# Kernel tuning notes

Measured on AMD Instinct MI355X. Metric: run time of the kernel, lower is better.

## Reference

```python
import jax, jax.numpy as jnp
import numpy as np

B, G = 64, 48            # events, grid side -> N = B*G*G nodes
N = B * G * G
DIMS = [128, 102, 73, 44, 16]   # channel schedule from GraphZ defaults
KERN = 3                 # GMM kernels on the conv layer
MAXV = 1.0               # Cartesian(max_value=neighbors=1)


def _build_graph():
    # 3x3 window graph (radius 1, self loops) per event, as in window_edges
    ix, iy = np.meshgrid(np.arange(G), np.arange(G), indexing='ij')
    ix, iy = ix.ravel(), iy.ravel()
    srcs, tgts = [], []
    for dx in (-1, 0, 1):
        for dy in (-1, 0, 1):
            jx, jy = ix + dx, iy + dy
            m = (jx >= 0) & (jx < G) & (jy >= 0) & (jy < G)
            srcs.append(jx[m] * G + jy[m])
            tgts.append(ix[m] * G + iy[m])
    src, tgt = np.concatenate(srcs), np.concatenate(tgts)
    base = (np.arange(B) * G * G)[:, None]
    ei = np.stack([(base + src[None]).ravel(), (base + tgt[None]).ravel()])
    pos = np.stack([np.tile(ix, B).astype(np.float32),
                    np.tile(iy, B).astype(np.float32),
                    np.repeat(np.arange(B), G * G).astype(np.float32)], axis=1)
    return ei.astype(np.int32), pos


def setup_inputs() -> dict:
    key = jax.random.key(0)
    ks = jax.random.split(key, 16)
    ei, pos = _build_graph()
    inp = {
        'x': jax.random.normal(ks[0], (N, DIMS[0]), jnp.float32),
        'pos': jnp.asarray(pos),
        'edge_index': jnp.asarray(ei),
    }
    # pointwise layer 0: 128->102 (+BN)
    inp['w0'] = jax.random.normal(ks[1], (DIMS[0], DIMS[1]), jnp.float32) * (1.0 / np.sqrt(DIMS[0]))
    inp['b0'] = jnp.zeros((DIMS[1],), jnp.float32)
    inp['gamma0'] = jnp.ones((DIMS[1],), jnp.float32)
    inp['beta0'] = jnp.zeros((DIMS[1],), jnp.float32)
    # pointwise layer 1: 102->73 (+BN)
    inp['w1'] = jax.random.normal(ks[2], (DIMS[1], DIMS[2]), jnp.float32) * (1.0 / np.sqrt(DIMS[1]))
    inp['b1'] = jnp.zeros((DIMS[2],), jnp.float32)
    inp['gamma1'] = jnp.ones((DIMS[2],), jnp.float32)
    inp['beta1'] = jnp.zeros((DIMS[2],), jnp.float32)
    # GMM conv layer 2: 73->44, 3 gaussian kernels (+BN)
    inp['w2'] = jax.random.normal(ks[3], (DIMS[2], DIMS[3]), jnp.float32) * (1.0 / np.sqrt(DIMS[2]))
    inp['g2'] = jax.random.normal(ks[4], (DIMS[2], KERN * DIMS[3]), jnp.float32) * (1.0 / np.sqrt(DIMS[2]))
    inp['mu2'] = jax.random.uniform(ks[5], (KERN, 2), jnp.float32)
    inp['sigma2'] = jax.random.uniform(ks[6], (KERN, 2), jnp.float32) + 0.5
    inp['b2'] = jnp.zeros((DIMS[3],), jnp.float32)
    inp['gamma2'] = jnp.ones((DIMS[3],), jnp.float32)
    inp['beta2'] = jnp.zeros((DIMS[3],), jnp.float32)
    # pointwise layer 3: 44->16
    inp['w3'] = jax.random.normal(ks[7], (DIMS[3], DIMS[4]), jnp.float32) * (1.0 / np.sqrt(DIMS[3]))
    inp['b3'] = jnp.zeros((DIMS[4],), jnp.float32)
    return inp


def _bn(x, gamma, beta):
    # BatchNorm1d training forward: biased batch stats over the node dim
    m = jnp.mean(x, axis=0)
    v = jnp.mean((x - m) ** 2, axis=0)
    return (x - m) * jax.lax.rsqrt(v + 1e-5) * gamma + beta


def _gmm_conv(x, ei, ea, g, mu, sigma, w_root, b, n):
    # PyG GMMConv (separate_gaussians=False, aggr='mean', root_weight, bias)
    E = ea.shape[0]
    kk = mu.shape[0]
    out = w_root.shape[1]
    xj = (x @ g)[ei[0]].reshape(E, kk, out)                 # gather transformed src feats
    gauss = jnp.exp(jnp.sum(-0.5 * (ea[:, None, :] - mu[None]) ** 2
                            / (1e-15 + sigma[None] ** 2), axis=-1))  # [E, K]
    msg = jnp.einsum('eko,ek->eo', xj, gauss)               # [E, out]
    s = jax.ops.segment_sum(msg, ei[1], num_segments=n)     # scatter-add to targets
    c = jax.ops.segment_sum(jnp.ones((E,), x.dtype), ei[1], num_segments=n)
    return s / jnp.maximum(c, 1.0)[:, None] + x @ w_root + b


def reference(x, pos, edge_index, w0, b0, gamma0, beta0, w1, b1, gamma1, beta1,
              w2, g2, mu2, sigma2, b2, gamma2, beta2, w3, b3):
    n = x.shape[0]
    pos2 = pos[:, :2]
    # Cartesian(max_value=1, norm=True): pseudo coords in [0, 1]
    ea = (pos2[edge_index[0]] - pos2[edge_index[1]]) / (2.0 * MAXV) + 0.5
    # layers 0,1: knn_graph(k=0) -> empty edge set -> GMMConv = root Linear + bias
    h = _bn(x @ w0 + b0, gamma0, beta0)
    h = _bn(h @ w1 + b1, gamma1, beta1)
    # layer 2: window-edge GMMConv with 3 gaussian kernels
    h = _bn(_gmm_conv(h, edge_index, ea, g2, mu2, sigma2, w2, b2, n), gamma2, beta2)
    # layer 3: pointwise, no norm
    return h @ w3 + b3
```

## Files before the change

### kernel.cpp

```cpp
#include <hip/hip_runtime.h>

#define GRIDW 48
#define NNODES 147456
#define NTILES 2304
#define GB 512

typedef __attribute__((ext_vector_type(8))) short short8;
typedef __attribute__((ext_vector_type(4))) float f32x4;
typedef __attribute__((ext_vector_type(4))) unsigned short ushort4v;

__device__ inline unsigned short f2bf(float f) {
    union { float f; unsigned u; } v; v.f = f;
    unsigned r = v.u + 0x7FFFu + ((v.u >> 16) & 1u);
    return (unsigned short)(r >> 16);
}
__device__ inline float bf2f(unsigned short h) {
    union { unsigned u; float f; } v; v.u = ((unsigned)h) << 16;
    return v.f;
}

__global__ void prep(const float* __restrict__ w0, const float* __restrict__ b0,
                     const float* __restrict__ w1, const float* __restrict__ b1,
                     const float* __restrict__ g2, const float* __restrict__ w2,
                     const float* __restrict__ b2, const float* __restrict__ w3,
                     const float* __restrict__ b3,
                     unsigned short* __restrict__ wt0, unsigned short* __restrict__ wt1,
                     unsigned short* __restrict__ wt2, unsigned short* __restrict__ wt3,
                     float* __restrict__ biasf0, float* __restrict__ biasf1,
                     float* __restrict__ biasf2, float* __restrict__ biasf3,
                     float* __restrict__ statz) {
    int id = blockIdx.x * 256 + threadIdx.x;
    if (id < 14336) {
        int col = id >> 7, k = id & 127;
        wt0[id] = (col < 102) ? f2bf(w0[k * 102 + col]) : (unsigned short)0;
    } else if (id < 24576) {
        int e = id - 14336; int col = e >> 7, k = e & 127;
        wt1[e] = (col < 73 && k < 102) ? f2bf(w1[k * 73 + col]) : (unsigned short)0;
    } else if (id < 41472) {
        int e = id - 24576; int col = e / 96, k = e - (e / 96) * 96;
        unsigned short v = 0;
        if (k < 73) v = (col < 132) ? f2bf(g2[k * 132 + col]) : f2bf(w2[k * 44 + (col - 132)]);
        wt2[e] = v;
    } else if (id < 42496) {
        int e = id - 41472; int col = e >> 6, k = e & 63;
        wt3[e] = (k < 44) ? f2bf(w3[k * 16 + col]) : (unsigned short)0;
    } else if (id < 42608) { int c = id - 42496; biasf0[c] = (c < 102) ? b0[c] : 0.f; }
    else if (id < 42688) { int c = id - 42608; biasf1[c] = (c < 73) ? b1[c] : 0.f; }
    else if (id < 42864) { int c = id - 42688; biasf2[c] = (c < 132) ? 0.f : b2[c - 132]; }
    else if (id < 42880) { int c = id - 42864; biasf3[c] = b3[c]; }
    else if (id < 43392) { statz[id - 42880] = 0.f; }
}

template<int K, int KP, int MP, int MOUT, int PREVM, int BNSRC,
         bool STATS, bool OUTBF, bool ABF16>
__global__ __launch_bounds__(256) void gemm_p(
    const void* __restrict__ Ain, const unsigned short* __restrict__ WT,
    const float* __restrict__ biasf,
    const float* __restrict__ q0, const float* __restrict__ q1,
    const float* __restrict__ q2, const float* __restrict__ q3,
    float invN, void* __restrict__ Yout,
    float* __restrict__ sumO, float* __restrict__ ssO)
{
    constexpr int KS = KP + 8;
    constexpr int NCF = MP / 16;
    constexpr int UPR = ABF16 ? (K / 8) : (K / 4);
    constexpr int TOT = 64 * UPR;
    constexpr int NLD = (TOT + 255) / 256;
    __shared__ __align__(16) unsigned short As[2][64 * KS];
    __shared__ __align__(16) unsigned short Bs[MP * KS];
    __shared__ float bnA[KP], bnB[KP];

    const int tid = threadIdx.x;
    const int lane = tid & 63, wv = tid >> 6, qd = lane >> 4, lc = lane & 15;

    if (BNSRC == 1) {
        if (tid < KP) {
            float a = 0.f, b = 0.f;
            if (tid < PREVM) {
                float m = q0[tid] * invN;
                float v = q1[tid] * invN - m * m;
                float sc = q2[tid] * rsqrtf(v + 1e-5f);
                a = sc; b = q3[tid] - m * sc;
            }
            bnA[tid] = a; bnB[tid] = b;
        }
    } else if (BNSRC == 2) {
        if (tid < KP) {
            bnA[tid] = (tid < PREVM) ? q0[tid] : 0.f;
            bnB[tid] = (tid < PREVM) ? q1[tid] : 0.f;
        }
    }
    for (int g = tid; g < MP * (KP / 8); g += 256) {
        int col = g / (KP / 8), u = g - col * (KP / 8);
        *(uint4*)&Bs[col * KS + u * 8] = *(const uint4*)&WT[(size_t)col * KP + u * 8];
    }
    if constexpr (KP > K) {
        constexpr int PADU = (KP - K) / 2;
        for (int g = tid; g < 64 * PADU; g += 256) {
            int row = g / PADU, u = g - row * PADU;
            *(unsigned*)&As[0][row * KS + K + u * 2] = 0u;
            *(unsigned*)&As[1][row * KS + K + u * 2] = 0u;
        }
    }

    float bvr[NCF];
#pragma unroll
    for (int cf = 0; cf < NCF; ++cf) bvr[cf] = biasf[cf * 16 + lc];

    float cs[NCF], cq[NCF];
    if (STATS) {
#pragma unroll
        for (int cf = 0; cf < NCF; ++cf) { cs[cf] = 0.f; cq[cf] = 0.f; }
    }

    uint4 pfb[NLD];
    float4 pff[NLD];

    int t = blockIdx.x;
#pragma unroll
    for (int i = 0; i < NLD; ++i) {
        int g = tid + 256 * i;
        if (g < TOT) {
            if constexpr (ABF16)
                pfb[i] = *(const uint4*)((const unsigned short*)Ain + (size_t)t * 64 * K + g * 8);
            else
                pff[i] = *(const float4*)((const float*)Ain + (size_t)t * 64 * K + g * 4);
        }
    }
    __syncthreads();

    int buf = 0;
    for (; t < NTILES; t += GB) {
#pragma unroll
        for (int i = 0; i < NLD; ++i) {
            int g = tid + 256 * i;
            if (g < TOT) {
                int row = g / UPR, u = g - row * UPR;
                if constexpr (ABF16) {
                    uint4 w = pfb[i];
                    if (BNSRC != 0) {
                        unsigned* wp = (unsigned*)&w;
#pragma unroll
                        for (int pp = 0; pp < 4; ++pp) {
                            int kk = u * 8 + 2 * pp;
                            float lo = bf2f((unsigned short)(wp[pp] & 0xFFFFu)) * bnA[kk] + bnB[kk];
                            float hi = bf2f((unsigned short)(wp[pp] >> 16)) * bnA[kk + 1] + bnB[kk + 1];
                            wp[pp] = (unsigned)f2bf(lo) | ((unsigned)f2bf(hi) << 16);
                        }
                    }
                    *(uint4*)&As[buf][row * KS + u * 8] = w;
                } else {
                    float4 v = pff[i];
                    if (BNSRC != 0) {
                        int kk = u * 4;
                        v.x = v.x * bnA[kk] + bnB[kk];
                        v.y = v.y * bnA[kk + 1] + bnB[kk + 1];
                        v.z = v.z * bnA[kk + 2] + bnB[kk + 2];
                        v.w = v.w * bnA[kk + 3] + bnB[kk + 3];
                    }
                    unsigned lo = (unsigned)f2bf(v.x) | ((unsigned)f2bf(v.y) << 16);
                    unsigned hi = (unsigned)f2bf(v.z) | ((unsigned)f2bf(v.w) << 16);
                    *(uint2*)&As[buf][row * KS + u * 4] = make_uint2(lo, hi);
                }
            }
        }
        int t2 = t + GB;
        if (t2 < NTILES) {
#pragma unroll
            for (int i = 0; i < NLD; ++i) {
                int g = tid + 256 * i;
                if (g < TOT) {
                    if constexpr (ABF16)
                        pfb[i] = *(const uint4*)((const unsigned short*)Ain + (size_t)t2 * 64 * K + g * 8);
                    else
                        pff[i] = *(const float4*)((const float*)Ain + (size_t)t2 * 64 * K + g * 4);
                }
            }
        }
        __syncthreads();

        f32x4 acc[NCF];
#pragma unroll
        for (int cf = 0; cf < NCF; ++cf) acc[cf] = (f32x4){0.f, 0.f, 0.f, 0.f};
#pragma unroll
        for (int kt = 0; kt < KP / 32; ++kt) {
            const int kb = kt * 32 + qd * 8;
            short8 a = *(const short8*)&As[buf][(wv * 16 + lc) * KS + kb];
#pragma unroll
            for (int cf = 0; cf < NCF; ++cf) {
                short8 b = *(const short8*)&Bs[(cf * 16 + lc) * KS + kb];
                acc[cf] = __builtin_amdgcn_mfma_f32_16x16x32_bf16(a, b, acc[cf], 0, 0, 0);
            }
        }
#pragma unroll
        for (int cf = 0; cf < NCF; ++cf) {
            const int col = cf * 16 + lc;
            const float bv = bvr[cf];
#pragma unroll
            for (int rr = 0; rr < 4; ++rr) {
                float v = acc[cf][rr] + bv;
                int row = t * 64 + wv * 16 + qd * 4 + rr;
                if (OUTBF) ((unsigned short*)Yout)[(size_t)row * MP + col] = f2bf(v);
                else       ((float*)Yout)[(size_t)row * MP + col] = v;
                if (STATS) { cs[cf] += v; cq[cf] += v * v; }
            }
        }
        buf ^= 1;
    }

    if (STATS) {
        __syncthreads();
        float* red = (float*)As;
        float* redq = red + 4 * MP;
#pragma unroll
        for (int cf = 0; cf < NCF; ++cf) {
            float s = cs[cf], qq = cq[cf];
            s += __shfl_down(s, 32, 64); s += __shfl_down(s, 16, 64);
            qq += __shfl_down(qq, 32, 64); qq += __shfl_down(qq, 16, 64);
            if (lane < 16) {
                red[wv * MP + cf * 16 + lane] = s;
                redq[wv * MP + cf * 16 + lane] = qq;
            }
        }
        __syncthreads();
        if (tid < MOUT) {
            float s = red[tid] + red[MP + tid] + red[2 * MP + tid] + red[3 * MP + tid];
            float qq = redq[tid] + redq[MP + tid] + redq[2 * MP + tid] + redq[3 * MP + tid];
            atomicAdd(&sumO[tid], s);
            atomicAdd(&ssO[tid], qq);
        }
    }
}

__global__ __launch_bounds__(256) void gmm_stencil(
    const unsigned short* __restrict__ TR, unsigned short* __restrict__ C,
    const float* __restrict__ mu, const float* __restrict__ sigma,
    float* __restrict__ sum2, float* __restrict__ ss2)
{
    __shared__ float gs[9][3];
    __shared__ float red[88];
    const int tid = threadIdx.x;
    if (tid < 88) red[tid] = 0.f;
    if (tid < 27) {
        int d = tid / 3, k = tid - (tid / 3) * 3;
        int dx = d / 3 - 1, dy = d % 3 - 1;
        float ex = 0.5f * dx + 0.5f, ey = 0.5f * dy + 0.5f;
        float mx = mu[k * 2], my = mu[k * 2 + 1];
        float sx = sigma[k * 2], sy = sigma[k * 2 + 1];
        gs[d][k] = expf(-0.5f * ((ex - mx) * (ex - mx) / (1e-15f + sx * sx) +
                                 (ey - my) * (ey - my) / (1e-15f + sy * sy)));
    }
    __syncthreads();

    const int r = blockIdx.x & 7;
    const int m = blockIdx.x >> 3;
    const int batch = r * 8 + (m >> 3);
    const int band = m & 7;
    const int base = batch * 2304 + band * 288;

    if (tid < 253) {
        const int og = tid % 11;
        const int ln0 = tid / 11;
        const int c0 = og * 4;
        float4 s4 = make_float4(0, 0, 0, 0), q4 = make_float4(0, 0, 0, 0);

        for (int i = 0; i < 13; ++i) {
            int ln = ln0 + 23 * i;
            if (ln >= 288) break;
            int node = base + ln;
            int rx = ln / 48, iy = ln - rx * 48;
            int ix = band * 6 + rx;
            float ax = 0, ay = 0, az = 0, aw = 0;
#pragma unroll
            for (int dx = -1; dx <= 1; ++dx) {
                int jx = ix + dx;
                if (jx < 0 || jx >= GRIDW) continue;
#pragma unroll
                for (int dy = -1; dy <= 1; ++dy) {
                    int jy = iy + dy;
                    if (jy < 0 || jy >= GRIDW) continue;
                    int d = (dx + 1) * 3 + (dy + 1);
                    const unsigned short* tj = TR + (size_t)(node + dx * GRIDW + dy) * 176 + c0;
                    float g0 = gs[d][0], g1 = gs[d][1], g2v = gs[d][2];
                    ushort4v t0 = *(const ushort4v*)tj;
                    ushort4v t1 = *(const ushort4v*)(tj + 44);
                    ushort4v t2 = *(const ushort4v*)(tj + 88);
                    ax += g0 * bf2f(t0.x) + g1 * bf2f(t1.x) + g2v * bf2f(t2.x);
                    ay += g0 * bf2f(t0.y) + g1 * bf2f(t1.y) + g2v * bf2f(t2.y);
                    az += g0 * bf2f(t0.z) + g1 * bf2f(t1.z) + g2v * bf2f(t2.z);
                    aw += g0 * bf2f(t0.w) + g1 * bf2f(t1.w) + g2v * bf2f(t2.w);
                }
            }
            int cnt = ((ix > 0) + (ix < GRIDW - 1) + 1) * ((iy > 0) + (iy < GRIDW - 1) + 1);
            float inv = 1.f / (float)cnt;
            const unsigned short* rp = TR + (size_t)node * 176 + 132 + c0;
            ushort4v rv = *(const ushort4v*)rp;
            float ox = ax * inv + bf2f(rv.x);
            float oy = ay * inv + bf2f(rv.y);
            float oz = az * inv + bf2f(rv.z);
            float ow = aw * inv + bf2f(rv.w);
            unsigned lo = (unsigned)f2bf(ox) | ((unsigned)f2bf(oy) << 16);
            unsigned hi = (unsigned)f2bf(oz) | ((unsigned)f2bf(ow) << 16);
            *(uint2*)&C[(size_t)node * 48 + c0] = make_uint2(lo, hi);
            if (og == 10)
                *(uint2*)&C[(size_t)node * 48 + 44] = make_uint2(0u, 0u);
            s4.x += ox; s4.y += oy; s4.z += oz; s4.w += ow;
            q4.x += ox * ox; q4.y += oy * oy; q4.z += oz * oz; q4.w += ow * ow;
        }
        atomicAdd(&red[c0 + 0], s4.x); atomicAdd(&red[c0 + 1], s4.y);
        atomicAdd(&red[c0 + 2], s4.z); atomicAdd(&red[c0 + 3], s4.w);
        atomicAdd(&red[44 + c0 + 0], q4.x); atomicAdd(&red[44 + c0 + 1], q4.y);
        atomicAdd(&red[44 + c0 + 2], q4.z); atomicAdd(&red[44 + c0 + 3], q4.w);
    }
    __syncthreads();
    if (tid < 44) atomicAdd(&sum2[tid], red[tid]);
    else if (tid < 88) atomicAdd(&ss2[tid - 44], red[tid]);
}

extern "C" void kernel_launch(void* const* d_in, const int* in_sizes, int n_in,
                              void* d_out, int out_size, void* d_ws, size_t ws_size,
                              hipStream_t stream) {
    const float* x      = (const float*)d_in[0];
    const float* w0     = (const float*)d_in[3];
    const float* b0     = (const float*)d_in[4];
    const float* gamma0 = (const float*)d_in[5];
    const float* beta0  = (const float*)d_in[6];
    const float* w1     = (const float*)d_in[7];
    const float* b1     = (const float*)d_in[8];
    const float* gamma1 = (const float*)d_in[9];
    const float* beta1  = (const float*)d_in[10];
    const float* w2     = (const float*)d_in[11];
    const float* g2     = (const float*)d_in[12];
    const float* mu2    = (const float*)d_in[13];
    const float* sigma2 = (const float*)d_in[14];
    const float* b2     = (const float*)d_in[15];
    const float* gamma2 = (const float*)d_in[16];
    const float* beta2  = (const float*)d_in[17];
    const float* w3     = (const float*)d_in[18];
    const float* b3     = (const float*)d_in[19];
    float* out = (float*)d_out;

    const int N = NNODES;
    const float invN = 1.0f / (float)N;

    const size_t tailOff = (size_t)N * 132;
    size_t need = (tailOff + 90000) * sizeof(float);
    if (ws_size < need) return;

    float* ws = (float*)d_ws;
    unsigned short* bufY1 = (unsigned short*)ws;
    unsigned short* bufC  = (unsigned short*)ws;
    unsigned short* bufY0 = (unsigned short*)(ws + (size_t)N * 44);
    unsigned short* bufTR = bufY0;

    float* tail = ws + tailOff;
    float* sum0 = tail;
    float* ss0  = tail + 112;
    float* sum1 = tail + 224;
    float* ss1  = tail + 304;
    float* sum2 = tail + 384;
    float* ss2  = tail + 448;
    float* biasf0 = tail + 512;
    float* biasf1 = tail + 624;
    float* biasf2 = tail + 704;
    float* biasf3 = tail + 880;
    unsigned short* wt0 = (unsigned short*)(tail + 896);
    unsigned short* wt1 = wt0 + 14336;
    unsigned short* wt2 = wt1 + 10240;
    unsigned short* wt3 = wt2 + 16896;

    prep<<<169, 256, 0, stream>>>(w0, b0, w1, b1, g2, w2, b2, w3, b3,
                                  wt0, wt1, wt2, wt3,
                                  biasf0, biasf1, biasf2, biasf3, tail);

    gemm_p<128, 128, 112, 102, 0, 0, true, true, false><<<GB, 256, 0, stream>>>(
        x, wt0, biasf0, nullptr, nullptr, nullptr, nullptr, invN, bufY0, sum0, ss0);

    gemm_p<112, 128, 80, 73, 102, 1, true, true, true><<<GB, 256, 0, stream>>>(
        bufY0, wt1, biasf1, sum0, ss0, gamma0, beta0, invN, bufY1, sum1, ss1);

    gemm_p<80, 96, 176, 176, 73, 1, false, true, true><<<GB, 256, 0, stream>>>(
        bufY1, wt2, biasf2, sum1, ss1, gamma1, beta1, invN, bufTR, nullptr, nullptr);

    gmm_stencil<<<512, 256, 0, stream>>>(bufTR, bufC, mu2, sigma2, sum2, ss2);

    gemm_p<48, 64, 16, 16, 44, 1, false, false, true><<<GB, 256, 0, stream>>>(
        bufC, wt3, biasf3, sum2, ss2, gamma2, beta2, invN, out, nullptr, nullptr);
}
```

Before: 267.0 us.

## Pad GMM transform blocks to 48 channels and vectorize stencil with 16-byte loads

```diff
diff --git a/kernel.cpp b/kernel.cpp
--- a/kernel.cpp
+++ b/kernel.cpp
@@ -7,7 +7,6 @@
 
 typedef __attribute__((ext_vector_type(8))) short short8;
 typedef __attribute__((ext_vector_type(4))) float f32x4;
-typedef __attribute__((ext_vector_type(4))) unsigned short ushort4v;
 
 __device__ inline unsigned short f2bf(float f) {
     union { float f; unsigned u; } v; v.f = f;
@@ -36,19 +35,22 @@
     } else if (id < 24576) {
         int e = id - 14336; int col = e >> 7, k = e & 127;
         wt1[e] = (col < 73 && k < 102) ? f2bf(w1[k * 73 + col]) : (unsigned short)0;
-    } else if (id < 41472) {
+    } else if (id < 43008) {
         int e = id - 24576; int col = e / 96, k = e - (e / 96) * 96;
+        int blk = col / 48, c = col - blk * 48;
         unsigned short v = 0;
-        if (k < 73) v = (col < 132) ? f2bf(g2[k * 132 + col]) : f2bf(w2[k * 44 + (col - 132)]);
+        if (k < 73 && c < 44)
+            v = (blk < 3) ? f2bf(g2[k * 132 + blk * 44 + c]) : f2bf(w2[k * 44 + c]);
         wt2[e] = v;
-    } else if (id < 42496) {
-        int e = id - 41472; int col = e >> 6, k = e & 63;
+    } else if (id < 44032) {
+        int e = id - 43008; int col = e >> 6, k = e & 63;
         wt3[e] = (k < 44) ? f2bf(w3[k * 16 + col]) : (unsigned short)0;
-    } else if (id < 42608) { int c = id - 42496; biasf0[c] = (c < 102) ? b0[c] : 0.f; }
-    else if (id < 42688) { int c = id - 42608; biasf1[c] = (c < 73) ? b1[c] : 0.f; }
-    else if (id < 42864) { int c = id - 42688; biasf2[c] = (c < 132) ? 0.f : b2[c - 132]; }
-    else if (id < 42880) { int c = id - 42864; biasf3[c] = b3[c]; }
-    else if (id < 43392) { statz[id - 42880] = 0.f; }
+    } else if (id < 44144) { int c = id - 44032; biasf0[c] = (c < 102) ? b0[c] : 0.f; }
+    else if (id < 44224) { int c = id - 44144; biasf1[c] = (c < 73) ? b1[c] : 0.f; }
+    else if (id < 44416) { int c = id - 44224; int blk = c / 48, cc = c - blk * 48;
+                           biasf2[c] = (blk == 3 && cc < 44) ? b2[cc] : 0.f; }
+    else if (id < 44432) { int c = id - 44416; biasf3[c] = b3[c]; }
+    else if (id < 44944) { statz[id - 44432] = 0.f; }
 }
 
 template<int K, int KP, int MP, int MOUT, int PREVM, int BNSRC,
@@ -232,15 +234,25 @@
     }
 }
 
-__global__ __launch_bounds__(256) void gmm_stencil(
+__device__ inline void fma8(const unsigned short* __restrict__ p, float g, float* acc) {
+    uint4 v = *(const uint4*)p;
+    unsigned w[4] = {v.x, v.y, v.z, v.w};
+#pragma unroll
+    for (int j = 0; j < 4; ++j) {
+        acc[2 * j]     += g * bf2f((unsigned short)(w[j] & 0xFFFFu));
+        acc[2 * j + 1] += g * bf2f((unsigned short)(w[j] >> 16));
+    }
+}
+
+__global__ __launch_bounds__(256, 4) void gmm_stencil(
     const unsigned short* __restrict__ TR, unsigned short* __restrict__ C,
     const float* __restrict__ mu, const float* __restrict__ sigma,
     float* __restrict__ sum2, float* __restrict__ ss2)
 {
     __shared__ float gs[9][3];
-    __shared__ float red[88];
+    __shared__ float red[96];
     const int tid = threadIdx.x;
-    if (tid < 88) red[tid] = 0.f;
+    if (tid < 96) red[tid] = 0.f;
     if (tid < 27) {
         int d = tid / 3, k = tid - (tid / 3) * 3;
         int dx = d / 3 - 1, dy = d % 3 - 1;
@@ -254,23 +266,26 @@
 
     const int r = blockIdx.x & 7;
     const int m = blockIdx.x >> 3;
-    const int batch = r * 8 + (m >> 3);
-    const int band = m & 7;
-    const int base = batch * 2304 + band * 288;
-
-    if (tid < 253) {
-        const int og = tid % 11;
-        const int ln0 = tid / 11;
-        const int c0 = og * 4;
-        float4 s4 = make_float4(0, 0, 0, 0), q4 = make_float4(0, 0, 0, 0);
-
-        for (int i = 0; i < 13; ++i) {
-            int ln = ln0 + 23 * i;
-            if (ln >= 288) break;
+    const int batch = r * 8 + (m >> 4);
+    const int band = m & 15;
+    const int base = batch * 2304 + band * 144;
+
+    const int og8 = tid % 6;
+    const int ln0 = tid / 6;
+    const int c0 = og8 * 8;
+
+    float s8[8] = {0, 0, 0, 0, 0, 0, 0, 0};
+    float q8[8] = {0, 0, 0, 0, 0, 0, 0, 0};
+
+    if (tid < 252) {
+#pragma unroll
+        for (int i = 0; i < 4; ++i) {
+            int ln = ln0 + 42 * i;
+            if (ln >= 144) break;
             int node = base + ln;
             int rx = ln / 48, iy = ln - rx * 48;
-            int ix = band * 6 + rx;
-            float ax = 0, ay = 0, az = 0, aw = 0;
+            int ix = band * 3 + rx;
+            float acc[8] = {0, 0, 0, 0, 0, 0, 0, 0};
 #pragma unroll
             for (int dx = -1; dx <= 1; ++dx) {
                 int jx = ix + dx;
@@ -280,41 +295,40 @@
                     int jy = iy + dy;
                     if (jy < 0 || jy >= GRIDW) continue;
                     int d = (dx + 1) * 3 + (dy + 1);
-                    const unsigned short* tj = TR + (size_t)(node + dx * GRIDW + dy) * 176 + c0;
-                    float g0 = gs[d][0], g1 = gs[d][1], g2v = gs[d][2];
-                    ushort4v t0 = *(const ushort4v*)tj;
-                    ushort4v t1 = *(const ushort4v*)(tj + 44);
-                    ushort4v t2 = *(const ushort4v*)(tj + 88);
-                    ax += g0 * bf2f(t0.x) + g1 * bf2f(t1.x) + g2v * bf2f(t2.x);
-                    ay += g0 * bf2f(t0.y) + g1 * bf2f(t1.y) + g2v * bf2f(t2.y);
-                    az += g0 * bf2f(t0.z) + g1 * bf2f(t1.z) + g2v * bf2f(t2.z);
-                    aw += g0 * bf2f(t0.w) + g1 * bf2f(t1.w) + g2v * bf2f(t2.w);
+                    const unsigned short* tj = TR + (size_t)(node + dx * GRIDW + dy) * 192 + c0;
+                    fma8(tj,      gs[d][0], acc);
+                    fma8(tj + 48, gs[d][1], acc);
+                    fma8(tj + 96, gs[d][2], acc);
                 }
             }
             int cnt = ((ix > 0) + (ix < GRIDW - 1) + 1) * ((iy > 0) + (iy < GRIDW - 1) + 1);
             float inv = 1.f / (float)cnt;
-            const unsigned short* rp = TR + (size_t)node * 176 + 132 + c0;
-            ushort4v rv = *(const ushort4v*)rp;
-            float ox = ax * inv + bf2f(rv.x);
-            float oy = ay * inv + bf2f(rv.y);
-            float oz = az * inv + bf2f(rv.z);
-            float ow = aw * inv + bf2f(rv.w);
-            unsigned lo = (unsigned)f2bf(ox) | ((unsigned)f2bf(oy) << 16);
-            unsigned hi = (unsigned)f2bf(oz) | ((unsigned)f2bf(ow) << 16);
-            *(uint2*)&C[(size_t)node * 48 + c0] = make_uint2(lo, hi);
-            if (og == 10)
-                *(uint2*)&C[(size_t)node * 48 + 44] = make_uint2(0u, 0u);
-            s4.x += ox; s4.y += oy; s4.z += oz; s4.w += ow;
-            q4.x += ox * ox; q4.y += oy * oy; q4.z += oz * oz; q4.w += ow * ow;
-        }
-        atomicAdd(&red[c0 + 0], s4.x); atomicAdd(&red[c0 + 1], s4.y);
-        atomicAdd(&red[c0 + 2], s4.z); atomicAdd(&red[c0 + 3], s4.w);
-        atomicAdd(&red[44 + c0 + 0], q4.x); atomicAdd(&red[44 + c0 + 1], q4.y);
-        atomicAdd(&red[44 + c0 + 2], q4.z); atomicAdd(&red[44 + c0 + 3], q4.w);
+            uint4 rv = *(const uint4*)(TR + (size_t)node * 192 + 144 + c0);
+            unsigned rw[4] = {rv.x, rv.y, rv.z, rv.w};
+            float o[8];
+#pragma unroll
+            for (int j = 0; j < 4; ++j) {
+                o[2 * j]     = acc[2 * j] * inv + bf2f((unsigned short)(rw[j] & 0xFFFFu));
+                o[2 * j + 1] = acc[2 * j + 1] * inv + bf2f((unsigned short)(rw[j] >> 16));
+            }
+            uint4 ov;
+            unsigned* op = (unsigned*)&ov;
+#pragma unroll
+            for (int j = 0; j < 4; ++j)
+                op[j] = (unsigned)f2bf(o[2 * j]) | ((unsigned)f2bf(o[2 * j + 1]) << 16);
+            *(uint4*)&C[(size_t)node * 48 + c0] = ov;
+#pragma unroll
+            for (int j = 0; j < 8; ++j) { s8[j] += o[j]; q8[j] += o[j] * o[j]; }
+        }
+    }
+#pragma unroll
+    for (int j = 0; j < 8; ++j) {
+        atomicAdd(&red[c0 + j], s8[j]);
+        atomicAdd(&red[48 + c0 + j], q8[j]);
     }
     __syncthreads();
     if (tid < 44) atomicAdd(&sum2[tid], red[tid]);
-    else if (tid < 88) atomicAdd(&ss2[tid - 44], red[tid]);
+    else if (tid >= 48 && tid < 92) atomicAdd(&ss2[tid - 48], red[tid]);
 }
 
 extern "C" void kernel_launch(void* const* d_in, const int* in_sizes, int n_in,
@@ -343,8 +357,8 @@
     const int N = NNODES;
     const float invN = 1.0f / (float)N;
 
-    const size_t tailOff = (size_t)N * 132;
-    size_t need = (tailOff + 90000) * sizeof(float);
+    const size_t tailOff = (size_t)N * 140;
+    size_t need = (tailOff + 48000) * sizeof(float);
     if (ws_size < need) return;
 
     float* ws = (float*)d_ws;
@@ -363,13 +377,13 @@
     float* biasf0 = tail + 512;
     float* biasf1 = tail + 624;
     float* biasf2 = tail + 704;
-    float* biasf3 = tail + 880;
-    unsigned short* wt0 = (unsigned short*)(tail + 896);
+    float* biasf3 = tail + 896;
+    unsigned short* wt0 = (unsigned short*)(tail + 912);
     unsigned short* wt1 = wt0 + 14336;
     unsigned short* wt2 = wt1 + 10240;
-    unsigned short* wt3 = wt2 + 16896;
-
-    prep<<<169, 256, 0, stream>>>(w0, b0, w1, b1, g2, w2, b2, w3, b3,
+    unsigned short* wt3 = wt2 + 18432;
+
+    prep<<<176, 256, 0, stream>>>(w0, b0, w1, b1, g2, w2, b2, w3, b3,
                                   wt0, wt1, wt2, wt3,
                                   biasf0, biasf1, biasf2, biasf3, tail);
 
@@ -379,10 +393,10 @@
     gemm_p<112, 128, 80, 73, 102, 1, true, true, true><<<GB, 256, 0, stream>>>(
         bufY0, wt1, biasf1, sum0, ss0, gamma0, beta0, invN, bufY1, sum1, ss1);
 
-    gemm_p<80, 96, 176, 176, 73, 1, false, true, true><<<GB, 256, 0, stream>>>(
+    gemm_p<80, 96, 192, 192, 73, 1, false, true, true><<<GB, 256, 0, stream>>>(
         bufY1, wt2, biasf2, sum1, ss1, gamma1, beta1, invN, bufTR, nullptr, nullptr);
 
-    gmm_stencil<<<512, 256, 0, stream>>>(bufTR, bufC, mu2, sigma2, sum2, ss2);
+    gmm_stencil<<<1024, 256, 0, stream>>>(bufTR, bufC, mu2, sigma2, sum2, ss2);
 
     gemm_p<48, 64, 16, 16, 44, 1, false, false, true><<<GB, 256, 0, stream>>>(
         bufC, wt3, biasf3, sum2, ss2, gamma2, beta2, invN, out, nullptr, nullptr);
```

Result: slower. 275.3 us (+3.1%).

## Factor Gaussian weights into separable x/y terms and slide column partials in stencil

Applied to the files above, without the earlier changes.

```diff
diff --git a/kernel.cpp b/kernel.cpp
--- a/kernel.cpp
+++ b/kernel.cpp
@@ -7,7 +7,6 @@
 
 typedef __attribute__((ext_vector_type(8))) short short8;
 typedef __attribute__((ext_vector_type(4))) float f32x4;
-typedef __attribute__((ext_vector_type(4))) unsigned short ushort4v;
 
 __device__ inline unsigned short f2bf(float f) {
     union { float f; unsigned u; } v; v.f = f;
@@ -232,85 +231,103 @@
     }
 }
 
+__device__ inline void load_u(const unsigned short* __restrict__ TR, int b,
+                              int jx, int iy, int c0, const float (*gy)[3],
+                              float* __restrict__ u) {
+#pragma unroll
+    for (int j = 0; j < 12; ++j) u[j] = 0.f;
+    if (jx < 0 || jx >= GRIDW) return;
+    const unsigned short* rowp = TR + (size_t)(b * 2304 + jx * 48) * 176;
+#pragma unroll
+    for (int dy = -1; dy <= 1; ++dy) {
+        int jy = iy + dy;
+        if (jy < 0 || jy >= GRIDW) continue;
+        const unsigned short* np = rowp + (size_t)jy * 176 + c0;
+#pragma unroll
+        for (int k = 0; k < 3; ++k) {
+            uint2 v = *(const uint2*)(np + k * 44);
+            float g = gy[dy + 1][k];
+            u[k * 4 + 0] += g * bf2f((unsigned short)(v.x & 0xFFFFu));
+            u[k * 4 + 1] += g * bf2f((unsigned short)(v.x >> 16));
+            u[k * 4 + 2] += g * bf2f((unsigned short)(v.y & 0xFFFFu));
+            u[k * 4 + 3] += g * bf2f((unsigned short)(v.y >> 16));
+        }
+    }
+}
+
 __global__ __launch_bounds__(256) void gmm_stencil(
     const unsigned short* __restrict__ TR, unsigned short* __restrict__ C,
     const float* __restrict__ mu, const float* __restrict__ sigma,
     float* __restrict__ sum2, float* __restrict__ ss2)
 {
-    __shared__ float gs[9][3];
+    __shared__ float gx[3][3], gy[3][3];
     __shared__ float red[88];
     const int tid = threadIdx.x;
     if (tid < 88) red[tid] = 0.f;
-    if (tid < 27) {
-        int d = tid / 3, k = tid - (tid / 3) * 3;
-        int dx = d / 3 - 1, dy = d % 3 - 1;
-        float ex = 0.5f * dx + 0.5f, ey = 0.5f * dy + 0.5f;
-        float mx = mu[k * 2], my = mu[k * 2 + 1];
-        float sx = sigma[k * 2], sy = sigma[k * 2 + 1];
-        gs[d][k] = expf(-0.5f * ((ex - mx) * (ex - mx) / (1e-15f + sx * sx) +
-                                 (ey - my) * (ey - my) / (1e-15f + sy * sy)));
+    if (tid < 18) {
+        int d = (tid / 3) % 3, k = tid % 3;
+        bool isy = tid >= 9;
+        float e = 0.5f * (float)(d - 1) + 0.5f;
+        float mm = mu[k * 2 + (isy ? 1 : 0)];
+        float sg = sigma[k * 2 + (isy ? 1 : 0)];
+        float v = expf(-0.5f * (e - mm) * (e - mm) / (1e-15f + sg * sg));
+        if (isy) gy[d][k] = v; else gx[d][k] = v;
     }
     __syncthreads();
 
     const int r = blockIdx.x & 7;
     const int m = blockIdx.x >> 3;
-    const int batch = r * 8 + (m >> 3);
-    const int band = m & 7;
-    const int base = batch * 2304 + band * 288;
-
-    if (tid < 253) {
-        const int og = tid % 11;
-        const int ln0 = tid / 11;
-        const int c0 = og * 4;
-        float4 s4 = make_float4(0, 0, 0, 0), q4 = make_float4(0, 0, 0, 0);
-
-        for (int i = 0; i < 13; ++i) {
-            int ln = ln0 + 23 * i;
-            if (ln >= 288) break;
-            int node = base + ln;
-            int rx = ln / 48, iy = ln - rx * 48;
-            int ix = band * 6 + rx;
-            float ax = 0, ay = 0, az = 0, aw = 0;
-#pragma unroll
-            for (int dx = -1; dx <= 1; ++dx) {
-                int jx = ix + dx;
-                if (jx < 0 || jx >= GRIDW) continue;
-#pragma unroll
-                for (int dy = -1; dy <= 1; ++dy) {
-                    int jy = iy + dy;
-                    if (jy < 0 || jy >= GRIDW) continue;
-                    int d = (dx + 1) * 3 + (dy + 1);
-                    const unsigned short* tj = TR + (size_t)(node + dx * GRIDW + dy) * 176 + c0;
-                    float g0 = gs[d][0], g1 = gs[d][1], g2v = gs[d][2];
-                    ushort4v t0 = *(const ushort4v*)tj;
-                    ushort4v t1 = *(const ushort4v*)(tj + 44);
-                    ushort4v t2 = *(const ushort4v*)(tj + 88);
-                    ax += g0 * bf2f(t0.x) + g1 * bf2f(t1.x) + g2v * bf2f(t2.x);
-                    ay += g0 * bf2f(t0.y) + g1 * bf2f(t1.y) + g2v * bf2f(t2.y);
-                    az += g0 * bf2f(t0.z) + g1 * bf2f(t1.z) + g2v * bf2f(t2.z);
-                    aw += g0 * bf2f(t0.w) + g1 * bf2f(t1.w) + g2v * bf2f(t2.w);
-                }
-            }
-            int cnt = ((ix > 0) + (ix < GRIDW - 1) + 1) * ((iy > 0) + (iy < GRIDW - 1) + 1);
-            float inv = 1.f / (float)cnt;
-            const unsigned short* rp = TR + (size_t)node * 176 + 132 + c0;
-            ushort4v rv = *(const ushort4v*)rp;
-            float ox = ax * inv + bf2f(rv.x);
-            float oy = ay * inv + bf2f(rv.y);
-            float oz = az * inv + bf2f(rv.z);
-            float ow = aw * inv + bf2f(rv.w);
-            unsigned lo = (unsigned)f2bf(ox) | ((unsigned)f2bf(oy) << 16);
-            unsigned hi = (unsigned)f2bf(oz) | ((unsigned)f2bf(ow) << 16);
+    const int b = r * 8 + (m >> 4);
+    const int x0 = (m & 15) * 3;
+
+    for (int p = 0; p < 3; ++p) {
+        int idx = tid + 256 * p;
+        if (idx >= 528) break;
+        int og = idx % 11, iy = idx / 11;
+        int c0 = og * 4;
+        float u0[12], u1[12], u2[12];
+        load_u(TR, b, x0 - 1, iy, c0, gy, u0);
+        load_u(TR, b, x0,     iy, c0, gy, u1);
+        float s4[4] = {0, 0, 0, 0}, q4[4] = {0, 0, 0, 0};
+        int ny = 1 + (iy > 0) + (iy < GRIDW - 1);
+#pragma unroll
+        for (int st = 0; st < 3; ++st) {
+            int ix = x0 + st;
+            float* ua = (st == 0) ? u0 : ((st == 1) ? u1 : u2);
+            float* ub = (st == 0) ? u1 : ((st == 1) ? u2 : u0);
+            float* uc = (st == 0) ? u2 : ((st == 1) ? u0 : u1);
+            load_u(TR, b, ix + 1, iy, c0, gy, uc);
+            int nx = 1 + (ix > 0) + (ix < GRIDW - 1);
+            float inv = 1.f / (float)(nx * ny);
+            int node = b * 2304 + ix * 48 + iy;
+            uint2 rv = *(const uint2*)(TR + (size_t)node * 176 + 132 + c0);
+            float o[4];
+#pragma unroll
+            for (int j = 0; j < 4; ++j) {
+                float acc = 0.f;
+#pragma unroll
+                for (int k = 0; k < 3; ++k)
+                    acc += gx[0][k] * ua[k * 4 + j] + gx[1][k] * ub[k * 4 + j]
+                         + gx[2][k] * uc[k * 4 + j];
+                o[j] = acc * inv;
+            }
+            o[0] += bf2f((unsigned short)(rv.x & 0xFFFFu));
+            o[1] += bf2f((unsigned short)(rv.x >> 16));
+            o[2] += bf2f((unsigned short)(rv.y & 0xFFFFu));
+            o[3] += bf2f((unsigned short)(rv.y >> 16));
+            unsigned lo = (unsigned)f2bf(o[0]) | ((unsigned)f2bf(o[1]) << 16);
+            unsigned hi = (unsigned)f2bf(o[2]) | ((unsigned)f2bf(o[3]) << 16);
             *(uint2*)&C[(size_t)node * 48 + c0] = make_uint2(lo, hi);
             if (og == 10)
                 *(uint2*)&C[(size_t)node * 48 + 44] = make_uint2(0u, 0u);
-            s4.x += ox; s4.y += oy; s4.z += oz; s4.w += ow;
-            q4.x += ox * ox; q4.y += oy * oy; q4.z += oz * oz; q4.w += ow * ow;
-        }
-        atomicAdd(&red[c0 + 0], s4.x); atomicAdd(&red[c0 + 1], s4.y);
-        atomicAdd(&red[c0 + 2], s4.z); atomicAdd(&red[c0 + 3], s4.w);
-        atomicAdd(&red[44 + c0 + 0], q4.x); atomicAdd(&red[44 + c0 + 1], q4.y);
-        atomicAdd(&red[44 + c0 + 2], q4.z); atomicAdd(&red[44 + c0 + 3], q4.w);
+#pragma unroll
+            for (int j = 0; j < 4; ++j) { s4[j] += o[j]; q4[j] += o[j] * o[j]; }
+        }
+#pragma unroll
+        for (int j = 0; j < 4; ++j) {
+            atomicAdd(&red[c0 + j], s4[j]);
+            atomicAdd(&red[44 + c0 + j], q4[j]);
+        }
     }
     __syncthreads();
     if (tid < 44) atomicAdd(&sum2[tid], red[tid]);
@@ -344,7 +361,7 @@
     const float invN = 1.0f / (float)N;
 
     const size_t tailOff = (size_t)N * 132;
-    size_t need = (tailOff + 90000) * sizeof(float);
+    size_t need = (tailOff + 48000) * sizeof(float);
     if (ws_size < need) return;
 
     float* ws = (float*)d_ws;
@@ -369,7 +386,7 @@
     unsigned short* wt2 = wt1 + 10240;
     unsigned short* wt3 = wt2 + 16896;
 
-    prep<<<169, 256, 0, stream>>>(w0, b0, w1, b1, g2, w2, b2, w3, b3,
+    prep<<<170, 256, 0, stream>>>(w0, b0, w1, b1, g2, w2, b2, w3, b3,
                                   wt0, wt1, wt2, wt3,
                                   biasf0, biasf1, biasf2, biasf3, tail);
 
@@ -382,7 +399,7 @@
     gemm_p<80, 96, 176, 176, 73, 1, false, true, true><<<GB, 256, 0, stream>>>(
         bufY1, wt2, biasf2, sum1, ss1, gamma1, beta1, invN, bufTR, nullptr, nullptr);
 
-    gmm_stencil<<<512, 256, 0, stream>>>(bufTR, bufC, mu2, sigma2, sum2, ss2);
+    gmm_stencil<<<1024, 256, 0, stream>>>(bufTR, bufC, mu2, sigma2, sum2, ss2);
 
     gemm_p<48, 64, 16, 16, 44, 1, false, false, true><<<GB, 256, 0, stream>>>(
         bufC, wt3, biasf3, sum2, ss2, gamma2, beta2, invN, out, nullptr, nullptr);
```

New measurement: 272.3 us. No clear change (+2.0%).
